# Optimization experiments

Hardware: AMD Instinct MI355X
Metric: run time of the kernel (lower is better)

## Reference

```python
import jax, jax.numpy as jnp
import numpy as np

D_MODEL = 1024
D_K = 64  # d_model // heads


def setup_inputs() -> dict:
    key = jax.random.key(0)
    ks = jax.random.split(key, 9)
    B, S = 8, 2048
    q = jax.random.normal(ks[0], (B, S, D_MODEL), dtype=jnp.float32)
    k = jax.random.normal(ks[1], (B, S, D_MODEL), dtype=jnp.float32)
    v = jax.random.normal(ks[2], (B, S, D_MODEL), dtype=jnp.float32)
    # Causal mask: True = blocked (masked_fill with -inf)
    mask = ~jnp.tril(jnp.ones((S, S), dtype=bool))
    # Linear params (stored as [in, out]); torch Linear init ~ U(-1/sqrt(in), 1/sqrt(in))
    lim = 1.0 / np.sqrt(D_MODEL)
    Wq = jax.random.uniform(ks[3], (D_MODEL, D_K), jnp.float32, -lim, lim)
    Wk = jax.random.uniform(ks[4], (D_MODEL, D_K), jnp.float32, -lim, lim)
    Wv = jax.random.uniform(ks[5], (D_MODEL, D_K), jnp.float32, -lim, lim)
    bq = jax.random.uniform(ks[6], (D_K,), jnp.float32, -lim, lim)
    bk = jax.random.uniform(ks[7], (D_K,), jnp.float32, -lim, lim)
    bv = jax.random.uniform(ks[8], (D_K,), jnp.float32, -lim, lim)
    return {"q": q, "k": k, "v": v, "mask": mask,
            "Wq": Wq, "bq": bq, "Wk": Wk, "bk": bk, "Wv": Wv, "bv": bv}


def reference(q, k, v, mask, Wq, bq, Wk, bk, Wv, bv):
    qp = q @ Wq + bq              # [B, S, d_k]
    kp = k @ Wk + bk              # [B, S, d_k]
    vp = v @ Wv + bv              # [B, S, d_k]
    scale = 1.0 / jnp.sqrt(jnp.float32(D_K))
    scores = jnp.einsum("bqd,bkd->bqk", qp, kp) * scale  # [B, S, S]
    scores = jnp.where(mask, -jnp.inf, scores)
    attn = jax.nn.softmax(scores, axis=-1)
    return jnp.einsum("bqk,bkd->bqd", attn, vp)  # [B, S, d_k]
```

## Files before the change

kernel.cpp:

```cpp
#include <hip/hip_runtime.h>
#include <hip/hip_bf16.h>

typedef short s4 __attribute__((ext_vector_type(4)));
typedef short s8 __attribute__((ext_vector_type(8)));
typedef float f4 __attribute__((ext_vector_type(4)));

#define MFMA16(a, b, c) __builtin_amdgcn_mfma_f32_16x16x16bf16_1k(a, b, c, 0, 0, 0)

__device__ __forceinline__ short f2bf(float f) {
    union { float f; unsigned u; } v; v.f = f;
    unsigned r = v.u + 0x7fffu + ((v.u >> 16) & 1u);
    return (short)(r >> 16);
}

struct ProjArgs {
    const float* X[3];
    const float* W[3];
    const float* b[3];
    unsigned short* O[3];
};

__global__ __launch_bounds__(256) void proj_kernel(ProjArgs args) {
    __shared__ short lA[64][68];
    __shared__ short lW[64][68];

    const int t  = threadIdx.x;
    const int wv = t >> 6, ln = t & 63, lg = ln >> 4, lr = ln & 15;
    const int which = blockIdx.y;

    const float* X = args.X[which] + (size_t)blockIdx.x * 64 * 1024;
    const float* W = args.W[which];

    f4 acc[4] = {f4{0,0,0,0}, f4{0,0,0,0}, f4{0,0,0,0}, f4{0,0,0,0}};

    for (int kk = 0; kk < 1024; kk += 64) {
        #pragma unroll
        for (int i = 0; i < 4; ++i) {
            int f  = t + i * 256;
            int r  = f >> 4;
            int c4 = f & 15;
            f4 a = *(const f4*)(X + (size_t)r * 1024 + kk + c4 * 4);
            f4 w = *(const f4*)(W + (size_t)(kk + r) * 64 + c4 * 4);
            s4 ab; ab[0]=f2bf(a[0]); ab[1]=f2bf(a[1]); ab[2]=f2bf(a[2]); ab[3]=f2bf(a[3]);
            s4 wb; wb[0]=f2bf(w[0]); wb[1]=f2bf(w[1]); wb[2]=f2bf(w[2]); wb[3]=f2bf(w[3]);
            *(s4*)&lA[r][c4 * 4] = ab;
            *(s4*)&lW[r][c4 * 4] = wb;
        }
        __syncthreads();

        #pragma unroll
        for (int ks = 0; ks < 4; ++ks) {
            s4 af = *(const s4*)&lA[wv * 16 + lr][ks * 16 + 4 * lg];
            #pragma unroll
            for (int nf = 0; nf < 4; ++nf) {
                s4 bf;
                #pragma unroll
                for (int e = 0; e < 4; ++e)
                    bf[e] = lW[ks * 16 + 4 * lg + e][nf * 16 + lr];
                acc[nf] = MFMA16(af, bf, acc[nf]);
            }
        }
        __syncthreads();
    }

    const float* bias = args.b[which];
    unsigned short* O = args.O[which];
    #pragma unroll
    for (int nf = 0; nf < 4; ++nf) {
        float bs = bias[nf * 16 + lr];
        int col = nf * 16 + lr;
        #pragma unroll
        for (int e = 0; e < 4; ++e) {
            int r = wv * 16 + 4 * lg + e;
            int grow = blockIdx.x * 64 + r;
            unsigned short val = (unsigned short)f2bf(acc[nf][e] + bs);
            if (which == 2) {
                size_t idx = (size_t)(grow >> 11) * 131072
                           + (size_t)((grow & 2047) >> 6) * 4096
                           + (size_t)col * 64 + (grow & 63);
                O[idx] = val;
            } else {
                O[(size_t)grow * 64 + col] = val;
            }
        }
    }
}

__global__ __launch_bounds__(512) void attn_kernel(const unsigned short* __restrict__ qp,
                                                   const unsigned short* __restrict__ kp,
                                                   const unsigned short* __restrict__ vpT,
                                                   float* __restrict__ out) {
    __shared__ short lK[2][2][64][72];
    __shared__ short lV[2][2][64][72];

    const int t    = threadIdx.x;
    const int wave = t >> 6, ln = t & 63, lg = ln >> 4, lr = ln & 15;
    const int half = wave >> 2, hw = wave & 3;
    const int b = blockIdx.y, qt = blockIdx.x;
    const int qrow = qt * 64 + hw * 16 + lr;
    const int h = (qt + 2) >> 1;

    const int g = t >> 7, gi = t & 127, ghalf = g >> 1;
    const bool isV = (g & 1) != 0;
    const unsigned short* tb = (isV ? vpT : kp) + (size_t)b * 131072;

    const unsigned short* qpb = qp + (size_t)b * 131072;
    s4 qf[4];
    #pragma unroll
    for (int ks = 0; ks < 4; ++ks)
        qf[ks] = *(const s4*)(qpb + (size_t)qrow * 64 + ks * 16 + 4 * lg);

    f4 accO[4] = {f4{0,0,0,0}, f4{0,0,0,0}, f4{0,0,0,0}, f4{0,0,0,0}};
    float m = -3e38f, lsum = 0.f;

    s8 stg[4];
    {
        const unsigned short* p = tb + (size_t)(ghalf ? h : 0) * 4096;
        #pragma unroll
        for (int i = 0; i < 4; ++i)
            stg[i] = *(const s8*)(p + (gi + 128 * i) * 8);
    }

    int buf = 0;
    for (int j = 0; j < h; ++j) {
        {
            short (*dst)[72] = isV ? lV[ghalf][buf] : lK[ghalf][buf];
            #pragma unroll
            for (int i = 0; i < 4; ++i) {
                int s = gi + 128 * i;
                *(s8*)&dst[s >> 3][(s & 7) * 8] = stg[i];
            }
        }
        __syncthreads();

        if (j + 1 < h) {
            const unsigned short* p = tb + (size_t)((ghalf ? h : 0) + j + 1) * 4096;
            #pragma unroll
            for (int i = 0; i < 4; ++i)
                stg[i] = *(const s8*)(p + (gi + 128 * i) * 8);
        }

        const int kt = (half ? h : 0) + j;
        if (kt <= qt) {
            f4 st[4];
            #pragma unroll
            for (int kf = 0; kf < 4; ++kf) {
                f4 a = f4{0,0,0,0};
                #pragma unroll
                for (int ks = 0; ks < 4; ++ks) {
                    s4 kfr = *(const s4*)&lK[half][buf][kf * 16 + lr][ks * 16 + 4 * lg];
                    a = MFMA16(kfr, qf[ks], a);
                }
                st[kf] = a;
            }

            const bool diag = (kt == qt);
            const int kbase = kt * 64;
            float smax = -3e38f;
            #pragma unroll
            for (int kf = 0; kf < 4; ++kf) {
                #pragma unroll
                for (int e = 0; e < 4; ++e) {
                    float s = st[kf][e] * 0.125f;
                    if (diag && (kbase + kf * 16 + 4 * lg + e > qrow)) s = -3e38f;
                    st[kf][e] = s;
                    smax = fmaxf(smax, s);
                }
            }
            smax = fmaxf(smax, __shfl_xor(smax, 16));
            smax = fmaxf(smax, __shfl_xor(smax, 32));

            float mnew  = fmaxf(m, smax);
            float scale = __expf(m - mnew);
            float psum  = 0.f;
            s4 pf[4];
            #pragma unroll
            for (int kf = 0; kf < 4; ++kf) {
                f4 p;
                #pragma unroll
                for (int e = 0; e < 4; ++e) { p[e] = __expf(st[kf][e] - mnew); psum += p[e]; }
                s4 pb; pb[0]=f2bf(p[0]); pb[1]=f2bf(p[1]); pb[2]=f2bf(p[2]); pb[3]=f2bf(p[3]);
                pf[kf] = pb;
            }
            psum += __shfl_xor(psum, 16);
            psum += __shfl_xor(psum, 32);
            lsum = lsum * scale + psum;
            m = mnew;
            #pragma unroll
            for (int df = 0; df < 4; ++df) accO[df] *= scale;

            #pragma unroll
            for (int df = 0; df < 4; ++df) {
                #pragma unroll
                for (int kf = 0; kf < 4; ++kf) {
                    s4 vf = *(const s4*)&lV[half][buf][df * 16 + lr][kf * 16 + 4 * lg];
                    accO[df] = MFMA16(vf, pf[kf], accO[df]);
                }
            }
        }
        buf ^= 1;
    }

    __syncthreads();
    float* ex = (float*)&lK[0][0][0][0];
    const int idx = (hw * 64 + ln) * 19;
    if (half == 1) {
        ex[idx + 0] = m;
        ex[idx + 1] = lsum;
        #pragma unroll
        for (int df = 0; df < 4; ++df)
            #pragma unroll
            for (int e = 0; e < 4; ++e)
                ex[idx + 2 + df * 4 + e] = accO[df][e];
    }
    __syncthreads();
    if (half == 0) {
        float mB = ex[idx + 0], lB = ex[idx + 1];
        float mx = fmaxf(m, mB);
        float sA = __expf(m - mx), sB = __expf(mB - mx);
        float linv = 1.f / (lsum * sA + lB * sB);
        float* ob = out + ((size_t)b * 2048 + qrow) * 64;
        #pragma unroll
        for (int df = 0; df < 4; ++df) {
            f4 o;
            #pragma unroll
            for (int e = 0; e < 4; ++e)
                o[e] = (accO[df][e] * sA + ex[idx + 2 + df * 4 + e] * sB) * linv;
            *(f4*)(ob + df * 16 + 4 * lg) = o;
        }
    }
}

extern "C" void kernel_launch(void* const* d_in, const int* in_sizes, int n_in,
                              void* d_out, int out_size, void* d_ws, size_t ws_size,
                              hipStream_t stream) {
    const float* q  = (const float*)d_in[0];
    const float* k  = (const float*)d_in[1];
    const float* v  = (const float*)d_in[2];
    const float* Wq = (const float*)d_in[4];
    const float* bq = (const float*)d_in[5];
    const float* Wk = (const float*)d_in[6];
    const float* bk = (const float*)d_in[7];
    const float* Wv = (const float*)d_in[8];
    const float* bv = (const float*)d_in[9];

    unsigned short* qp  = (unsigned short*)d_ws;
    unsigned short* kp  = qp + (size_t)16384 * 64;
    unsigned short* vpT = kp + (size_t)16384 * 64;

    ProjArgs pa;
    pa.X[0] = q;  pa.X[1] = k;  pa.X[2] = v;
    pa.W[0] = Wq; pa.W[1] = Wk; pa.W[2] = Wv;
    pa.b[0] = bq; pa.b[1] = bk; pa.b[2] = bv;
    pa.O[0] = qp; pa.O[1] = kp; pa.O[2] = vpT;
    proj_kernel<<<dim3(256, 3), 256, 0, stream>>>(pa);

    attn_kernel<<<dim3(32, 8), 512, 0, stream>>>(qp, kp, vpT, (float*)d_out);
}
```

Before: 77.20 us.

## Split attention into 32-row query blocks with 256-thread workgroups

```diff
diff --git a/kernel.cpp b/kernel.cpp
--- a/kernel.cpp
+++ b/kernel.cpp
@@ -86,7 +86,7 @@
     }
 }
 
-__global__ __launch_bounds__(512) void attn_kernel(const unsigned short* __restrict__ qp,
+__global__ __launch_bounds__(256) void attn_kernel(const unsigned short* __restrict__ qp,
                                                    const unsigned short* __restrict__ kp,
                                                    const unsigned short* __restrict__ vpT,
                                                    float* __restrict__ out) {
@@ -95,14 +95,15 @@
 
     const int t    = threadIdx.x;
     const int wave = t >> 6, ln = t & 63, lg = ln >> 4, lr = ln & 15;
-    const int half = wave >> 2, hw = wave & 3;
-    const int b = blockIdx.y, qt = blockIdx.x;
-    const int qrow = qt * 64 + hw * 16 + lr;
-    const int h = (qt + 2) >> 1;
-
-    const int g = t >> 7, gi = t & 127, ghalf = g >> 1;
-    const bool isV = (g & 1) != 0;
-    const unsigned short* tb = (isV ? vpT : kp) + (size_t)b * 131072;
+    const int strip = wave >> 1, half = wave & 1;
+    const int b = blockIdx.y, g = blockIdx.x;
+    const int qrow = g * 32 + strip * 16 + lr;
+    const int P = (g >> 1) + 1;
+    const int h = (P + 1) >> 1;
+
+    const int sHalf = wave >> 1;
+    const bool sIsV = (wave & 1) != 0;
+    const unsigned short* tb = (sIsV ? vpT : kp) + (size_t)b * 131072;
 
     const unsigned short* qpb = qp + (size_t)b * 131072;
     s4 qf[4];
@@ -113,35 +114,35 @@
     f4 accO[4] = {f4{0,0,0,0}, f4{0,0,0,0}, f4{0,0,0,0}, f4{0,0,0,0}};
     float m = -3e38f, lsum = 0.f;
 
-    s8 stg[4];
+    s8 stg[8];
     {
-        const unsigned short* p = tb + (size_t)(ghalf ? h : 0) * 4096;
-        #pragma unroll
-        for (int i = 0; i < 4; ++i)
-            stg[i] = *(const s8*)(p + (gi + 128 * i) * 8);
+        const unsigned short* p = tb + (size_t)(sHalf ? h : 0) * 4096;
+        #pragma unroll
+        for (int i = 0; i < 8; ++i)
+            stg[i] = *(const s8*)(p + (ln + 64 * i) * 8);
     }
 
     int buf = 0;
     for (int j = 0; j < h; ++j) {
         {
-            short (*dst)[72] = isV ? lV[ghalf][buf] : lK[ghalf][buf];
-            #pragma unroll
-            for (int i = 0; i < 4; ++i) {
-                int s = gi + 128 * i;
+            short (*dst)[72] = sIsV ? lV[sHalf][buf] : lK[sHalf][buf];
+            #pragma unroll
+            for (int i = 0; i < 8; ++i) {
+                int s = ln + 64 * i;
                 *(s8*)&dst[s >> 3][(s & 7) * 8] = stg[i];
             }
         }
         __syncthreads();
 
         if (j + 1 < h) {
-            const unsigned short* p = tb + (size_t)((ghalf ? h : 0) + j + 1) * 4096;
-            #pragma unroll
-            for (int i = 0; i < 4; ++i)
-                stg[i] = *(const s8*)(p + (gi + 128 * i) * 8);
+            const unsigned short* p = tb + (size_t)((sHalf ? h : 0) + j + 1) * 4096;
+            #pragma unroll
+            for (int i = 0; i < 8; ++i)
+                stg[i] = *(const s8*)(p + (ln + 64 * i) * 8);
         }
 
         const int kt = (half ? h : 0) + j;
-        if (kt <= qt) {
+        if (kt < P) {
             f4 st[4];
             #pragma unroll
             for (int kf = 0; kf < 4; ++kf) {
@@ -154,7 +155,7 @@
                 st[kf] = a;
             }
 
-            const bool diag = (kt == qt);
+            const bool diag = (kt == P - 1);
             const int kbase = kt * 64;
             float smax = -3e38f;
             #pragma unroll
@@ -203,7 +204,7 @@
 
     __syncthreads();
     float* ex = (float*)&lK[0][0][0][0];
-    const int idx = (hw * 64 + ln) * 19;
+    const int idx = (strip * 64 + ln) * 18;
     if (half == 1) {
         ex[idx + 0] = m;
         ex[idx + 1] = lsum;
@@ -255,5 +256,5 @@
     pa.O[0] = qp; pa.O[1] = kp; pa.O[2] = vpT;
     proj_kernel<<<dim3(256, 3), 256, 0, stream>>>(pa);
 
-    attn_kernel<<<dim3(32, 8), 512, 0, stream>>>(qp, kp, vpT, (float*)d_out);
-}
+    attn_kernel<<<dim3(64, 8), 256, 0, stream>>>(qp, kp, vpT, (float*)d_out);
+}
```

Result: slower. 81.55 us (+5.6%).

## Split each key tile across waves instead of query rows in causal attention

Applied to the files above, without the earlier changes.

```diff
diff --git a/kernel.cpp b/kernel.cpp
--- a/kernel.cpp
+++ b/kernel.cpp
@@ -90,41 +90,50 @@
                                                    const unsigned short* __restrict__ kp,
                                                    const unsigned short* __restrict__ vpT,
                                                    float* __restrict__ out) {
-    __shared__ short lK[2][2][64][72];
-    __shared__ short lV[2][2][64][72];
+    __shared__ short lK[2][2][64][70];
+    __shared__ short lV[2][2][64][70];
 
     const int t    = threadIdx.x;
-    const int wave = t >> 6, ln = t & 63, lg = ln >> 4, lr = ln & 15;
-    const int half = wave >> 2, hw = wave & 3;
+    const int w    = t >> 6, ln = t & 63, lg = ln >> 4, lr = ln & 15;
+    const int sub  = w >> 2, sl = w & 3;
     const int b = blockIdx.y, qt = blockIdx.x;
-    const int qrow = qt * 64 + hw * 16 + lr;
-    const int h = (qt + 2) >> 1;
-
-    const int g = t >> 7, gi = t & 127, ghalf = g >> 1;
-    const bool isV = (g & 1) != 0;
+    const int niter = (qt >> 1) + 1;
+
+    const int g = t >> 7, gi = t & 127, gsub = g & 1;
+    const bool isV = g >= 2;
     const unsigned short* tb = (isV ? vpT : kp) + (size_t)b * 131072;
 
     const unsigned short* qpb = qp + (size_t)b * 131072;
-    s4 qf[4];
+    s4 qf_r[4][4];
     #pragma unroll
-    for (int ks = 0; ks < 4; ++ks)
-        qf[ks] = *(const s4*)(qpb + (size_t)qrow * 64 + ks * 16 + 4 * lg);
-
-    f4 accO[4] = {f4{0,0,0,0}, f4{0,0,0,0}, f4{0,0,0,0}, f4{0,0,0,0}};
-    float m = -3e38f, lsum = 0.f;
+    for (int qf = 0; qf < 4; ++qf)
+        #pragma unroll
+        for (int ks = 0; ks < 4; ++ks)
+            qf_r[qf][ks] = *(const s4*)(qpb + (size_t)(qt * 64 + 16 * qf + lr) * 64
+                                            + 16 * ks + 4 * lg);
+
+    f4 accO[4][4];
+    #pragma unroll
+    for (int df = 0; df < 4; ++df)
+        #pragma unroll
+        for (int qf = 0; qf < 4; ++qf) accO[df][qf] = f4{0,0,0,0};
+    float m[4] = {-3e38f, -3e38f, -3e38f, -3e38f};
+    float l[4] = {0.f, 0.f, 0.f, 0.f};
+
+    const float C = 0.125f * 1.44269504f;
 
     s8 stg[4];
     {
-        const unsigned short* p = tb + (size_t)(ghalf ? h : 0) * 4096;
+        const unsigned short* p = tb + (size_t)gsub * 4096;
         #pragma unroll
         for (int i = 0; i < 4; ++i)
             stg[i] = *(const s8*)(p + (gi + 128 * i) * 8);
     }
 
     int buf = 0;
-    for (int j = 0; j < h; ++j) {
+    for (int j = 0; j < niter; ++j) {
         {
-            short (*dst)[72] = isV ? lV[ghalf][buf] : lK[ghalf][buf];
+            short (*dst)[70] = isV ? lV[buf][gsub] : lK[buf][gsub];
             #pragma unroll
             for (int i = 0; i < 4; ++i) {
                 int s = gi + 128 * i;
@@ -133,101 +142,152 @@
         }
         __syncthreads();
 
-        if (j + 1 < h) {
-            const unsigned short* p = tb + (size_t)((ghalf ? h : 0) + j + 1) * 4096;
+        if (j + 1 < niter) {
+            const unsigned short* p = tb + (size_t)(2 * (j + 1) + gsub) * 4096;
             #pragma unroll
             for (int i = 0; i < 4; ++i)
                 stg[i] = *(const s8*)(p + (gi + 128 * i) * 8);
         }
 
-        const int kt = (half ? h : 0) + j;
-        if (kt <= qt) {
+        const int myTile = 2 * j + sub;
+        if (myTile <= qt) {
+            s4 kfr[4];
+            #pragma unroll
+            for (int ks = 0; ks < 4; ++ks)
+                kfr[ks] = *(const s4*)&lK[buf][sub][16 * sl + lr][16 * ks + 4 * lg];
+
             f4 st[4];
             #pragma unroll
-            for (int kf = 0; kf < 4; ++kf) {
+            for (int qf = 0; qf < 4; ++qf) {
                 f4 a = f4{0,0,0,0};
                 #pragma unroll
-                for (int ks = 0; ks < 4; ++ks) {
-                    s4 kfr = *(const s4*)&lK[half][buf][kf * 16 + lr][ks * 16 + 4 * lg];
-                    a = MFMA16(kfr, qf[ks], a);
+                for (int ks = 0; ks < 4; ++ks)
+                    a = MFMA16(kfr[ks], qf_r[qf][ks], a);
+                st[qf] = a;
+            }
+
+            const bool diag = (myTile == qt);
+            const int kbase = myTile * 64 + 16 * sl + 4 * lg;
+            float pmax[4];
+            #pragma unroll
+            for (int qf = 0; qf < 4; ++qf) {
+                f4 s2;
+                #pragma unroll
+                for (int e = 0; e < 4; ++e) {
+                    float s = st[qf][e] * C;
+                    if (diag && (kbase + e > qt * 64 + 16 * qf + lr)) s = -1e30f;
+                    s2[e] = s;
                 }
-                st[kf] = a;
-            }
-
-            const bool diag = (kt == qt);
-            const int kbase = kt * 64;
-            float smax = -3e38f;
-            #pragma unroll
-            for (int kf = 0; kf < 4; ++kf) {
-                #pragma unroll
-                for (int e = 0; e < 4; ++e) {
-                    float s = st[kf][e] * 0.125f;
-                    if (diag && (kbase + kf * 16 + 4 * lg + e > qrow)) s = -3e38f;
-                    st[kf][e] = s;
-                    smax = fmaxf(smax, s);
+                st[qf] = s2;
+                float mx = fmaxf(fmaxf(s2[0], s2[1]), fmaxf(s2[2], s2[3]));
+                mx = fmaxf(mx, __shfl_xor(mx, 16));
+                mx = fmaxf(mx, __shfl_xor(mx, 32));
+                pmax[qf] = mx;
+            }
+
+            float grow = fmaxf(fmaxf(pmax[0] - m[0], pmax[1] - m[1]),
+                               fmaxf(pmax[2] - m[2], pmax[3] - m[3]));
+            if (!__all(grow <= 8.0f)) {
+                #pragma unroll
+                for (int qf = 0; qf < 4; ++qf) {
+                    float mn = fmaxf(m[qf], pmax[qf]);
+                    float sc = __builtin_amdgcn_exp2f(m[qf] - mn);
+                    l[qf] *= sc;
+                    m[qf] = mn;
+                    #pragma unroll
+                    for (int df = 0; df < 4; ++df) accO[df][qf] *= sc;
                 }
             }
-            smax = fmaxf(smax, __shfl_xor(smax, 16));
-            smax = fmaxf(smax, __shfl_xor(smax, 32));
-
-            float mnew  = fmaxf(m, smax);
-            float scale = __expf(m - mnew);
-            float psum  = 0.f;
-            s4 pf[4];
-            #pragma unroll
-            for (int kf = 0; kf < 4; ++kf) {
+
+            s4 pb[4];
+            #pragma unroll
+            for (int qf = 0; qf < 4; ++qf) {
                 f4 p;
                 #pragma unroll
-                for (int e = 0; e < 4; ++e) { p[e] = __expf(st[kf][e] - mnew); psum += p[e]; }
-                s4 pb; pb[0]=f2bf(p[0]); pb[1]=f2bf(p[1]); pb[2]=f2bf(p[2]); pb[3]=f2bf(p[3]);
-                pf[kf] = pb;
-            }
-            psum += __shfl_xor(psum, 16);
-            psum += __shfl_xor(psum, 32);
-            lsum = lsum * scale + psum;
-            m = mnew;
-            #pragma unroll
-            for (int df = 0; df < 4; ++df) accO[df] *= scale;
+                for (int e = 0; e < 4; ++e)
+                    p[e] = __builtin_amdgcn_exp2f(st[qf][e] - m[qf]);
+                float ps = (p[0] + p[1]) + (p[2] + p[3]);
+                ps += __shfl_xor(ps, 16);
+                ps += __shfl_xor(ps, 32);
+                l[qf] += ps;
+                s4 pc; pc[0]=f2bf(p[0]); pc[1]=f2bf(p[1]); pc[2]=f2bf(p[2]); pc[3]=f2bf(p[3]);
+                pb[qf] = pc;
+            }
 
             #pragma unroll
             for (int df = 0; df < 4; ++df) {
-                #pragma unroll
-                for (int kf = 0; kf < 4; ++kf) {
-                    s4 vf = *(const s4*)&lV[half][buf][df * 16 + lr][kf * 16 + 4 * lg];
-                    accO[df] = MFMA16(vf, pf[kf], accO[df]);
-                }
+                s4 vf = *(const s4*)&lV[buf][sub][16 * df + lr][16 * sl + 4 * lg];
+                #pragma unroll
+                for (int qf = 0; qf < 4; ++qf)
+                    accO[df][qf] = MFMA16(vf, pb[qf], accO[df][qf]);
             }
         }
         buf ^= 1;
     }
 
     __syncthreads();
-    float* ex = (float*)&lK[0][0][0][0];
-    const int idx = (hw * 64 + ln) * 19;
-    if (half == 1) {
-        ex[idx + 0] = m;
-        ex[idx + 1] = lsum;
-        #pragma unroll
-        for (int df = 0; df < 4; ++df)
-            #pragma unroll
-            for (int e = 0; e < 4; ++e)
-                ex[idx + 2 + df * 4 + e] = accO[df][e];
+    float* arena = (float*)&lK[0][0][0][0];
+    float* ml   = arena;
+    float* Linv = arena + 1024;
+    float* Oacc = arena + 1152;
+
+    if (lg == 0) {
+        #pragma unroll
+        for (int qf = 0; qf < 4; ++qf) {
+            int idx = ((w * 4 + qf) * 16 + lr) * 2;
+            ml[idx] = m[qf];
+            ml[idx + 1] = l[qf];
+        }
     }
     __syncthreads();
-    if (half == 0) {
-        float mB = ex[idx + 0], lB = ex[idx + 1];
-        float mx = fmaxf(m, mB);
-        float sA = __expf(m - mx), sB = __expf(mB - mx);
-        float linv = 1.f / (lsum * sA + lB * sB);
-        float* ob = out + ((size_t)b * 2048 + qrow) * 64;
-        #pragma unroll
-        for (int df = 0; df < 4; ++df) {
-            f4 o;
-            #pragma unroll
-            for (int e = 0; e < 4; ++e)
-                o[e] = (accO[df][e] * sA + ex[idx + 2 + df * 4 + e] * sB) * linv;
-            *(f4*)(ob + df * 16 + 4 * lg) = o;
-        }
+
+    float scOwn[4];
+    {
+        #pragma unroll
+        for (int qf = 0; qf < 4; ++qf) {
+            float M = -3e38f;
+            #pragma unroll
+            for (int w2 = 0; w2 < 8; ++w2)
+                M = fmaxf(M, ml[((w2 * 4 + qf) * 16 + lr) * 2]);
+            float L = 0.f;
+            #pragma unroll
+            for (int w2 = 0; w2 < 8; ++w2) {
+                int idx = ((w2 * 4 + qf) * 16 + lr) * 2;
+                L += __builtin_amdgcn_exp2f(ml[idx] - M) * ml[idx + 1];
+            }
+            scOwn[qf] = __builtin_amdgcn_exp2f(m[qf] - M);
+            if (w == 0 && lg == 0) Linv[16 * qf + lr] = 1.f / L;
+        }
+    }
+    __syncthreads();
+
+    for (int step = 0; step < 8; ++step) {
+        if (w == step) {
+            #pragma unroll
+            for (int df = 0; df < 4; ++df)
+                #pragma unroll
+                for (int qf = 0; qf < 4; ++qf)
+                    #pragma unroll
+                    for (int e = 0; e < 4; ++e) {
+                        int idx = (16 * df + 4 * lg + e) * 66 + 16 * qf + lr;
+                        float v = scOwn[qf] * accO[df][qf][e];
+                        if (step == 0) Oacc[idx] = v; else Oacc[idx] += v;
+                    }
+        }
+        __syncthreads();
+    }
+
+    {
+        int row = t >> 3, c8 = t & 7;
+        float li = Linv[row];
+        float* ob = out + ((size_t)b * 2048 + qt * 64 + row) * 64 + c8 * 8;
+        f4 o0, o1;
+        #pragma unroll
+        for (int i = 0; i < 4; ++i) o0[i] = Oacc[(c8 * 8 + i) * 66 + row] * li;
+        #pragma unroll
+        for (int i = 0; i < 4; ++i) o1[i] = Oacc[(c8 * 8 + 4 + i) * 66 + row] * li;
+        *(f4*)ob = o0;
+        *(f4*)(ob + 4) = o1;
     }
 }
 
```

After: 90.05 us. 16.7% more time.

## Split causal attention KV range across two blocks per query tile with merge kernel

Applied to the files above, without the earlier changes.

```diff
diff --git a/kernel.cpp b/kernel.cpp
--- a/kernel.cpp
+++ b/kernel.cpp
@@ -86,19 +86,25 @@
     }
 }
 
-__global__ __launch_bounds__(512) void attn_kernel(const unsigned short* __restrict__ qp,
-                                                   const unsigned short* __restrict__ kp,
-                                                   const unsigned short* __restrict__ vpT,
-                                                   float* __restrict__ out) {
+__global__ __launch_bounds__(512) void attn_part(const unsigned short* __restrict__ qp,
+                                                 const unsigned short* __restrict__ kp,
+                                                 const unsigned short* __restrict__ vpT,
+                                                 float* __restrict__ partO,
+                                                 float* __restrict__ partML) {
     __shared__ short lK[2][2][64][72];
     __shared__ short lV[2][2][64][72];
 
     const int t    = threadIdx.x;
     const int wave = t >> 6, ln = t & 63, lg = ln >> 4, lr = ln & 15;
     const int half = wave >> 2, hw = wave & 3;
-    const int b = blockIdx.y, qt = blockIdx.x;
+    const int b = blockIdx.y, x = blockIdx.x;
+    const int qt = 31 - (x >> 1), z = x & 1;
+    const int P = qt + 1;
+    const int c = (P + 1) >> 1;
+    const int base  = z ? c : 0;
+    const int chunk = z ? (P - c) : c;
+    const int hA = (chunk + 1) >> 1;
     const int qrow = qt * 64 + hw * 16 + lr;
-    const int h = (qt + 2) >> 1;
 
     const int g = t >> 7, gi = t & 127, ghalf = g >> 1;
     const bool isV = (g & 1) != 0;
@@ -115,14 +121,14 @@
 
     s8 stg[4];
     {
-        const unsigned short* p = tb + (size_t)(ghalf ? h : 0) * 4096;
+        const unsigned short* p = tb + (size_t)(base + (ghalf ? hA : 0)) * 4096;
         #pragma unroll
         for (int i = 0; i < 4; ++i)
             stg[i] = *(const s8*)(p + (gi + 128 * i) * 8);
     }
 
     int buf = 0;
-    for (int j = 0; j < h; ++j) {
+    for (int j = 0; j < hA; ++j) {
         {
             short (*dst)[72] = isV ? lV[ghalf][buf] : lK[ghalf][buf];
             #pragma unroll
@@ -133,15 +139,15 @@
         }
         __syncthreads();
 
-        if (j + 1 < h) {
-            const unsigned short* p = tb + (size_t)((ghalf ? h : 0) + j + 1) * 4096;
+        if (j + 1 < hA) {
+            const unsigned short* p = tb + (size_t)(base + (ghalf ? hA : 0) + j + 1) * 4096;
             #pragma unroll
             for (int i = 0; i < 4; ++i)
                 stg[i] = *(const s8*)(p + (gi + 128 * i) * 8);
         }
 
-        const int kt = (half ? h : 0) + j;
-        if (kt <= qt) {
+        const int kt = base + (half ? hA : 0) + j;
+        if (kt < base + chunk) {
             f4 st[4];
             #pragma unroll
             for (int kf = 0; kf < 4; ++kf) {
@@ -218,16 +224,52 @@
         float mB = ex[idx + 0], lB = ex[idx + 1];
         float mx = fmaxf(m, mB);
         float sA = __expf(m - mx), sB = __expf(mB - mx);
-        float linv = 1.f / (lsum * sA + lB * sB);
-        float* ob = out + ((size_t)b * 2048 + qrow) * 64;
+        float lP = lsum * sA + lB * sB;
+
+        const size_t pidx = ((size_t)b * 32 + qt) * 2 + z;
+        float* Od = partO + pidx * 4096;
+        const int q = hw * 16 + lr;
         #pragma unroll
         for (int df = 0; df < 4; ++df) {
             f4 o;
             #pragma unroll
             for (int e = 0; e < 4; ++e)
-                o[e] = (accO[df][e] * sA + ex[idx + 2 + df * 4 + e] * sB) * linv;
-            *(f4*)(ob + df * 16 + 4 * lg) = o;
-        }
+                o[e] = accO[df][e] * sA + ex[idx + 2 + df * 4 + e] * sB;
+            *(f4*)(Od + (size_t)q * 64 + df * 16 + 4 * lg) = o;
+        }
+        if (lg == 0) {
+            partML[pidx * 128 + q * 2 + 0] = mx;
+            partML[pidx * 128 + q * 2 + 1] = lP;
+        }
+    }
+}
+
+__global__ __launch_bounds__(256) void attn_merge(const float* __restrict__ partO,
+                                                  const float* __restrict__ partML,
+                                                  float* __restrict__ out) {
+    const int t = threadIdx.x;
+    const int g = blockIdx.x, b = blockIdx.y;
+    const int q = t >> 2, dq = t & 3;
+
+    const size_t p0 = ((size_t)b * 32 + g) * 2;
+    const size_t p1 = p0 + 1;
+    float m0 = partML[p0 * 128 + q * 2], l0 = partML[p0 * 128 + q * 2 + 1];
+    float m1 = partML[p1 * 128 + q * 2], l1 = partML[p1 * 128 + q * 2 + 1];
+    float M  = fmaxf(m0, m1);
+    float s0 = __expf(m0 - M), s1 = __expf(m1 - M);
+    float inv = 1.f / (l0 * s0 + l1 * s1);
+
+    const float* O0 = partO + p0 * 4096 + (size_t)q * 64 + dq * 16;
+    const float* O1 = partO + p1 * 4096 + (size_t)q * 64 + dq * 16;
+    float* ob = out + ((size_t)b * 2048 + g * 64 + q) * 64 + dq * 16;
+    #pragma unroll
+    for (int i = 0; i < 4; ++i) {
+        f4 a = *(const f4*)(O0 + 4 * i);
+        f4 c = *(const f4*)(O1 + 4 * i);
+        f4 o;
+        #pragma unroll
+        for (int e = 0; e < 4; ++e) o[e] = (a[e] * s0 + c[e] * s1) * inv;
+        *(f4*)(ob + 4 * i) = o;
     }
 }
 
@@ -247,6 +289,8 @@
     unsigned short* qp  = (unsigned short*)d_ws;
     unsigned short* kp  = qp + (size_t)16384 * 64;
     unsigned short* vpT = kp + (size_t)16384 * 64;
+    float* partO  = (float*)(vpT + (size_t)16384 * 64);
+    float* partML = partO + (size_t)512 * 4096;
 
     ProjArgs pa;
     pa.X[0] = q;  pa.X[1] = k;  pa.X[2] = v;
@@ -255,5 +299,6 @@
     pa.O[0] = qp; pa.O[1] = kp; pa.O[2] = vpT;
     proj_kernel<<<dim3(256, 3), 256, 0, stream>>>(pa);
 
-    attn_kernel<<<dim3(32, 8), 512, 0, stream>>>(qp, kp, vpT, (float*)d_out);
-}
+    attn_part<<<dim3(64, 8), 512, 0, stream>>>(qp, kp, vpT, partO, partML);
+    attn_merge<<<dim3(32, 8), 256, 0, stream>>>(partO, partML, (float*)d_out);
+}
```

New measurement: 78.67 us. No clear change (+1.9%).
